# Kernel optimization log

Hardware: AMD Instinct MI355X
Metric: run time of the kernel (lower is better)

Reference implementation:

```python
import jax, jax.numpy as jnp
import numpy as np

DIM = 384
NH = 16
HD = DIM // NH          # 24
HID = DIM * 4           # titan/cms hidden
RD = 2 * (HD // 3 // 2) # 8 rope channels per axis (d/h/w), 3*RD == HD


def _ln(x, scale, bias):
    m = x.mean(-1, keepdims=True)
    v = ((x - m) ** 2).mean(-1, keepdims=True)
    return (x - m) * jax.lax.rsqrt(v + 1e-5) * scale + bias


def _mlp(x, w1, b1, w2, b2):
    # TitanMemory / CMS level: Linear -> GELU -> Linear (titan_layers=2)
    h = jax.nn.gelu(x @ w1 + b1, approximate=False)
    return h @ w2 + b2


def _rotate(x, pos):
    # rotate_queries_or_keys: interleaved rotary. x: [B,nh,N,d], pos: [N]
    d = x.shape[-1]
    inv_freq = 1.0 / (10000.0 ** (jnp.arange(0, d, 2, dtype=jnp.float32) / d))
    ang = pos[:, None] * inv_freq[None, :]              # [N, d/2]
    sin, cos = jnp.sin(ang), jnp.cos(ang)
    x1, x2 = x[..., 0::2], x[..., 1::2]
    y1 = x1 * cos - x2 * sin
    y2 = x1 * sin + x2 * cos
    return jnp.stack([y1, y2], axis=-1).reshape(x.shape)


def _rope3d(q, T, H, W):
    # 3D RoPE on frame tokens (action_tokens=0): time / height / width axes
    B, N, D = q.shape
    qh = q.reshape(B, N, NH, HD).transpose(0, 2, 1, 3)   # [B,nh,N,hd]
    ids = jnp.arange(T * H * W)
    tpos = (ids // (H * W)).astype(jnp.float32)
    hpos = ((ids % (H * W)) // W).astype(jnp.float32)
    wpos = (ids % W).astype(jnp.float32)
    qd = _rotate(qh[..., :RD], tpos)
    qhh = _rotate(qh[..., RD:2 * RD], hpos)
    qww = _rotate(qh[..., 2 * RD:3 * RD], wpos)
    out = jnp.concatenate([qd, qhh, qww], axis=-1)
    return out.transpose(0, 2, 1, 3).reshape(B, N, D)


def setup_inputs() -> dict:
    key = jax.random.key(0)
    ks = jax.random.split(key, 8)
    B, T, H, W = 8, 8, 16, 16
    N = T * H * W
    p = lambda k, sh: jax.random.normal(k, sh, jnp.float32) * 0.02
    return {
        "x": jax.random.normal(ks[0], (B, N, DIM), jnp.float32),
        "norm1_scale": jnp.ones((DIM,), jnp.float32),
        "norm1_bias": jnp.zeros((DIM,), jnp.float32),
        "norm2_scale": jnp.ones((DIM,), jnp.float32),
        "norm2_bias": jnp.zeros((DIM,), jnp.float32),
        "q_w": p(ks[1], (DIM, DIM)),
        # stacked Titan memories: [M_k, M_v, M_eta, M_alpha, M_memory]
        "titan_w1": p(ks[2], (5, DIM, HID)),
        "titan_b1": jnp.zeros((5, HID), jnp.float32),
        "titan_w2": p(ks[3], (5, HID, DIM)),
        "titan_b2": jnp.zeros((5, DIM), jnp.float32),
        "out_w": p(ks[4], (DIM, DIM)),
        "out_b": jnp.zeros((DIM,), jnp.float32),
        # CMS levels: [fast, medium, slow]
        "cms_w1": p(ks[5], (3, DIM, HID)),
        "cms_b1": jnp.zeros((3, HID), jnp.float32),
        "cms_w2": p(ks[6], (3, HID, DIM)),
        "cms_b2": jnp.zeros((3, DIM), jnp.float32),
        "T": T, "H": H, "W": W, "action_tokens": 0,
    }


def reference(x, norm1_scale, norm1_bias, norm2_scale, norm2_bias, q_w,
              titan_w1, titan_b1, titan_w2, titan_b2, out_w, out_b,
              cms_w1, cms_b1, cms_w2, cms_b2, T, H, W, action_tokens):
    # Phase A: self-modifying Titan (eval path: retrieval only)
    y = _ln(x, norm1_scale, norm1_bias)
    q = y @ q_w                                  # static query projection (Eq. 76)
    q = _rope3d(q, T, H, W)                      # 3D RoPE (action_tokens == 0)
    out = _mlp(q, titan_w1[4], titan_b1[4], titan_w2[4], titan_b2[4])  # M_memory(q)
    out = out @ out_w + out_b                    # out_proj
    x = x + out                                  # residual (drop_path = identity)
    # Phase B: CMS multi-frequency MLP cascade
    y = _ln(x, norm2_scale, norm2_bias)
    cms = sum(_mlp(y, cms_w1[i], cms_b1[i], cms_w2[i], cms_b2[i]) for i in range(3))
    return x + cms
```

## Files before the change

### kernel.cpp

```cpp
#include <hip/hip_runtime.h>
#include <math.h>

typedef unsigned short u16;
typedef unsigned int u32;
typedef __attribute__((ext_vector_type(8))) short short8;
typedef __attribute__((ext_vector_type(4))) float f32x4;

#define DIM 384
#define HID 1536

static __device__ __forceinline__ float bf2f(u32 b){ return __uint_as_float(b << 16); }
static __device__ __forceinline__ u16 f2bf(float f){
  u32 u = __float_as_uint(f);
  u32 r = (u + 0x7fffu + ((u >> 16) & 1u)) >> 16;
  return (u16)r;
}
static __device__ __forceinline__ float gelu_fast(float v){
  float u = v * fmaf(0.0713548162726f, v * v, 1.59576912161f);
  float e = __builtin_amdgcn_exp2f(-1.44269504089f * u);
  return v * __builtin_amdgcn_rcpf(1.0f + e);
}
static __device__ __forceinline__ void gload_lds16(const u16* g, u16* l){
  __builtin_amdgcn_global_load_lds(
      (__attribute__((address_space(1))) void*)(void*)const_cast<u16*>(g),
      (__attribute__((address_space(3))) void*)(void*)l, 16, 0, 0);
}

__global__ __launch_bounds__(256) void ln_kernel(const float* __restrict__ x,
    const float* __restrict__ sc, const float* __restrict__ bi, u16* __restrict__ y){
  int lane = threadIdx.x & 63;
  int row = blockIdx.x * 4 + (threadIdx.x >> 6);
  const float* xr = x + (size_t)row * DIM;
  float v[6];
  float s = 0.f, sq = 0.f;
#pragma unroll
  for (int i = 0; i < 6; ++i){
    float f = xr[lane + 64*i];
    v[i] = f; s += f; sq += f*f;
  }
#pragma unroll
  for (int o = 1; o < 64; o <<= 1){ s += __shfl_xor(s, o); sq += __shfl_xor(sq, o); }
  float mean = s * (1.0f/DIM);
  float var = sq * (1.0f/DIM) - mean*mean;
  float inv = rsqrtf(var + 1e-5f);
  u16* yr = y + (size_t)row * DIM;
#pragma unroll
  for (int i = 0; i < 6; ++i){
    int c = lane + 64*i;
    yr[c] = f2bf((v[i] - mean) * inv * sc[c] + bi[c]);
  }
}

__global__ __launch_bounds__(256) void rope_kernel(u16* __restrict__ q,
    const int* __restrict__ Tp, const int* __restrict__ Hp, const int* __restrict__ Wp,
    int Mtok){
  int idx = blockIdx.x * 256 + threadIdx.x;
  int tok = idx / 192;
  if (tok >= Mtok) return;
  int p = idx - tok * 192;
  int H = *Hp, W = *Wp, T = *Tp;
  int HW = H * W;
  int Ns = T * HW;
  int n = tok % Ns;
  int head = p / 12;
  int pp = p - head * 12;
  int s = pp >> 2, f = pp & 3;
  float pos;
  if (s == 0)      pos = (float)(n / HW);
  else if (s == 1) pos = (float)((n / W) % H);
  else             pos = (float)(n % W);
  const float LOG2_10000 = 13.28771237954945f;
  float inv = __builtin_amdgcn_exp2f(-0.25f * (float)f * LOG2_10000);
  float ang = pos * inv;
  float sn = __sinf(ang), cs = __cosf(ang);
  size_t base = (size_t)tok * DIM + head * 24 + s * 8 + 2 * f;
  u32 u = *(u32*)(q + base);
  float x1 = bf2f(u & 0xffffu), x2 = bf2f(u >> 16);
  float y1 = x1 * cs - x2 * sn;
  float y2 = x1 * sn + x2 * cs;
  *(u32*)(q + base) = (u32)f2bf(y1) | ((u32)f2bf(y2) << 16);
}

template<int R, int C>
__global__ __launch_bounds__(256) void transpose_kernel(
    const float* __restrict__ s0, const float* __restrict__ s1,
    const float* __restrict__ s2, const float* __restrict__ s3,
    u16* __restrict__ d0, u16* __restrict__ d1, u16* __restrict__ d2, u16* __restrict__ d3,
    int dstStride){
  const float* src = (blockIdx.z == 0) ? s0 : (blockIdx.z == 1) ? s1 : (blockIdx.z == 2) ? s2 : s3;
  u16* dst         = (blockIdx.z == 0) ? d0 : (blockIdx.z == 1) ? d1 : (blockIdx.z == 2) ? d2 : d3;
  __shared__ u16 t[32][33];
  int tx = threadIdx.x & 31, ty = threadIdx.x >> 5;
  int r0 = blockIdx.y * 32, c0 = blockIdx.x * 32;
#pragma unroll
  for (int i = 0; i < 4; ++i)
    t[ty + 8*i][tx] = f2bf(src[(size_t)(r0 + ty + 8*i) * C + c0 + tx]);
  __syncthreads();
#pragma unroll
  for (int i = 0; i < 4; ++i)
    dst[(size_t)(c0 + ty + 8*i) * dstStride + r0 + tx] = t[tx][ty + 8*i];
}

__global__ void bias3_kernel(const float* __restrict__ b, float* __restrict__ o){
  int n = threadIdx.x;
  o[n] = b[n] + b[384 + n] + b[768 + n];
}

enum { E_NONE = 0, E_BIAS = 1, E_RES_F32 = 3, E_FINAL = 5 };

template<int BM, int N, int K, int EPI>
__global__ __launch_bounds__(256) void gemm_kernel(
    const u16* __restrict__ A, const u16* __restrict__ Bt,
    void* __restrict__ Cv, const float* __restrict__ bias,
    const float* __restrict__ res, float* __restrict__ accbuf){
  constexpr int BN = 128, BK = 64;
  constexpr int MT = BM / 32, NT = 4;
  constexpr int AIT = BM / 32, BIT = 4;
  __shared__ __align__(16) u16 As[BM * BK];
  __shared__ __align__(16) u16 Bs[BN * BK];
  const int tid = threadIdx.x;
  const int lane = tid & 63;
  const int wv = tid >> 6;
  const int wm = (wv >> 1) * (BM / 2);
  const int wn = (wv & 1) * 64;
  const int quad = lane >> 4;
  const int l16 = lane & 15;
  const int rsw = l16 & 7;
  const size_t m0 = (size_t)blockIdx.x * BM;
  const int n0 = blockIdx.y * BN;
  const int srow = lane >> 3;
  const int scol = ((lane & 7) ^ srow) * 8;

  f32x4 acc[MT][NT];
  const f32x4 zero = {0.f, 0.f, 0.f, 0.f};
#pragma unroll
  for (int mt = 0; mt < MT; ++mt)
#pragma unroll
    for (int nt = 0; nt < NT; ++nt) acc[mt][nt] = zero;

  for (int kt = 0; kt < K; kt += BK){
#pragma unroll
    for (int i = 0; i < AIT; ++i){
      int seg = i * 4 + wv;
      gload_lds16(A + (m0 + (size_t)(seg * 8 + srow)) * K + kt + scol, As + seg * 512);
    }
#pragma unroll
    for (int i = 0; i < BIT; ++i){
      int seg = i * 4 + wv;
      gload_lds16(Bt + (size_t)(n0 + seg * 8 + srow) * K + kt + scol, Bs + seg * 512);
    }
    __syncthreads();
#pragma unroll
    for (int kk = 0; kk < 2; ++kk){
      short8 af[MT], bfr[NT];
#pragma unroll
      for (int mt = 0; mt < MT; ++mt)
        af[mt] = *(const short8*)(As + (wm + mt*16 + l16) * BK + (((kk*4 + quad) ^ rsw) << 3));
#pragma unroll
      for (int nt = 0; nt < NT; ++nt)
        bfr[nt] = *(const short8*)(Bs + (wn + nt*16 + l16) * BK + (((kk*4 + quad) ^ rsw) << 3));
#pragma unroll
      for (int mt = 0; mt < MT; ++mt)
#pragma unroll
        for (int nt = 0; nt < NT; ++nt)
          acc[mt][nt] = __builtin_amdgcn_mfma_f32_16x16x32_bf16(af[mt], bfr[nt], acc[mt][nt], 0, 0, 0);
    }
    __syncthreads();
  }

#pragma unroll
  for (int mt = 0; mt < MT; ++mt){
#pragma unroll
    for (int nt = 0; nt < NT; ++nt){
      int ncol = n0 + wn + nt*16 + l16;
      float bv = (EPI != E_NONE) ? bias[ncol] : 0.f;
      size_t mbase = m0 + wm + mt*16 + quad*4;
#pragma unroll
      for (int r = 0; r < 4; ++r){
        size_t off = (mbase + r) * N + ncol;
        float vv = acc[mt][nt][r];
        if      (EPI == E_NONE)      ((u16*)Cv)[off] = f2bf(vv);
        else if (EPI == E_BIAS)      ((u16*)Cv)[off] = f2bf(vv + bv);
        else          accbuf[off] = vv + bv + res[off];
      }
    }
  }
}

template<int N, int K>
__global__ __launch_bounds__(512, 4) void gemm_up2_kernel(
    const u16* __restrict__ A, const u16* __restrict__ Bt,
    u16* __restrict__ C, const float* __restrict__ bias){
  constexpr int BK = 64;
  __shared__ __align__(16) u16 As[128 * BK];
  __shared__ __align__(16) u16 Bs[256 * BK];
  const int tid = threadIdx.x;
  const int lane = tid & 63;
  const int wv = tid >> 6;
  const int wm = (wv >> 1) * 32;
  const int wn = (wv & 1) * 128;
  const int quad = lane >> 4;
  const int l16 = lane & 15;
  const int rsw = l16 & 7;
  const size_t m0 = (size_t)blockIdx.x * 128;
  const int n0 = blockIdx.y * 256;
  const int srow = lane >> 3;
  const int scol = ((lane & 7) ^ srow) * 8;

  f32x4 acc[2][8];
  const f32x4 zero = {0.f, 0.f, 0.f, 0.f};
#pragma unroll
  for (int mt = 0; mt < 2; ++mt)
#pragma unroll
    for (int nt = 0; nt < 8; ++nt) acc[mt][nt] = zero;

  for (int kt = 0; kt < K; kt += BK){
#pragma unroll
    for (int i = 0; i < 2; ++i){
      int seg = i * 8 + wv;
      gload_lds16(A + (m0 + (size_t)(seg * 8 + srow)) * K + kt + scol, As + seg * 512);
    }
#pragma unroll
    for (int i = 0; i < 4; ++i){
      int seg = i * 8 + wv;
      gload_lds16(Bt + (size_t)(n0 + seg * 8 + srow) * K + kt + scol, Bs + seg * 512);
    }
    __syncthreads();
#pragma unroll
    for (int kk = 0; kk < 2; ++kk){
      short8 af[2], bfr[8];
#pragma unroll
      for (int mt = 0; mt < 2; ++mt)
        af[mt] = *(const short8*)(As + (wm + mt*16 + l16) * BK + (((kk*4 + quad) ^ rsw) << 3));
#pragma unroll
      for (int nt = 0; nt < 8; ++nt)
        bfr[nt] = *(const short8*)(Bs + (wn + nt*16 + l16) * BK + (((kk*4 + quad) ^ rsw) << 3));
#pragma unroll
      for (int mt = 0; mt < 2; ++mt)
#pragma unroll
        for (int nt = 0; nt < 8; ++nt)
          acc[mt][nt] = __builtin_amdgcn_mfma_f32_16x16x32_bf16(af[mt], bfr[nt], acc[mt][nt], 0, 0, 0);
    }
    __syncthreads();
  }

#pragma unroll
  for (int mt = 0; mt < 2; ++mt){
#pragma unroll
    for (int nt = 0; nt < 8; ++nt){
      int ncol = n0 + wn + nt*16 + l16;
      float bv = bias[ncol];
      size_t mbase = m0 + wm + mt*16 + quad*4;
#pragma unroll
      for (int r = 0; r < 4; ++r)
        C[(mbase + r) * N + ncol] = f2bf(gelu_fast(acc[mt][nt][r] + bv));
    }
  }
}

template<int N, int K, int EPI>
__global__ __launch_bounds__(512, 4) void gemm2_kernel(
    const u16* __restrict__ A, const u16* __restrict__ Bt,
    void* __restrict__ Cv, const float* __restrict__ bias,
    const float* __restrict__ accbuf){
  constexpr int BK = 64;
  __shared__ __align__(16) u16 As[128 * BK];
  __shared__ __align__(16) u16 Bs[128 * BK];
  const int tid = threadIdx.x;
  const int lane = tid & 63;
  const int wv = tid >> 6;
  const int wm = (wv >> 1) * 32;
  const int wn = (wv & 1) * 64;
  const int quad = lane >> 4;
  const int l16 = lane & 15;
  const int rsw = l16 & 7;
  const size_t m0 = (size_t)blockIdx.x * 128;
  const int n0 = blockIdx.y * 128;
  const int srow = lane >> 3;
  const int scol = ((lane & 7) ^ srow) * 8;

  f32x4 acc[2][4];
  const f32x4 zero = {0.f, 0.f, 0.f, 0.f};
#pragma unroll
  for (int mt = 0; mt < 2; ++mt)
#pragma unroll
    for (int nt = 0; nt < 4; ++nt) acc[mt][nt] = zero;

  for (int kt = 0; kt < K; kt += BK){
#pragma unroll
    for (int i = 0; i < 2; ++i){
      int seg = i * 8 + wv;
      gload_lds16(A + (m0 + (size_t)(seg * 8 + srow)) * K + kt + scol, As + seg * 512);
      gload_lds16(Bt + (size_t)(n0 + seg * 8 + srow) * K + kt + scol, Bs + seg * 512);
    }
    __syncthreads();
#pragma unroll
    for (int kk = 0; kk < 2; ++kk){
      short8 af[2], bfr[4];
#pragma unroll
      for (int mt = 0; mt < 2; ++mt)
        af[mt] = *(const short8*)(As + (wm + mt*16 + l16) * BK + (((kk*4 + quad) ^ rsw) << 3));
#pragma unroll
      for (int nt = 0; nt < 4; ++nt)
        bfr[nt] = *(const short8*)(Bs + (wn + nt*16 + l16) * BK + (((kk*4 + quad) ^ rsw) << 3));
#pragma unroll
      for (int mt = 0; mt < 2; ++mt)
#pragma unroll
        for (int nt = 0; nt < 4; ++nt)
          acc[mt][nt] = __builtin_amdgcn_mfma_f32_16x16x32_bf16(af[mt], bfr[nt], acc[mt][nt], 0, 0, 0);
    }
    __syncthreads();
  }

#pragma unroll
  for (int mt = 0; mt < 2; ++mt){
#pragma unroll
    for (int nt = 0; nt < 4; ++nt){
      int ncol = n0 + wn + nt*16 + l16;
      float bv = bias[ncol];
      size_t mbase = m0 + wm + mt*16 + quad*4;
#pragma unroll
      for (int r = 0; r < 4; ++r){
        size_t off = (mbase + r) * N + ncol;
        float vv = acc[mt][nt][r] + bv;
        if (EPI == E_BIAS) ((u16*)Cv)[off] = f2bf(vv);
        else  ((float*)Cv)[off] = accbuf[off] + vv;
      }
    }
  }
}

extern "C" void kernel_launch(void* const* d_in, const int* in_sizes, int n_in,
                              void* d_out, int out_size, void* d_ws, size_t ws_size,
                              hipStream_t stream) {
  const int W11 = DIM * HID;
  const float* x   = (const float*)d_in[0];
  const float* n1s = (const float*)d_in[1];
  const float* n1b = (const float*)d_in[2];
  const float* n2s = (const float*)d_in[3];
  const float* n2b = (const float*)d_in[4];
  const float* qw  = (const float*)d_in[5];
  const float* tw1 = (const float*)d_in[6] + 4 * W11;
  const float* tb1 = (const float*)d_in[7] + 4 * HID;
  const float* tw2 = (const float*)d_in[8] + 4 * W11;
  const float* tb2 = (const float*)d_in[9] + 4 * DIM;
  const float* ow  = (const float*)d_in[10];
  const float* ob  = (const float*)d_in[11];
  const float* cw1 = (const float*)d_in[12];
  const float* cb1 = (const float*)d_in[13];
  const float* cw2 = (const float*)d_in[14];
  const float* cb2 = (const float*)d_in[15];
  const int* Tp = (const int*)d_in[16];
  const int* Hp = (const int*)d_in[17];
  const int* Wp = (const int*)d_in[18];
  const int M = in_sizes[0] / DIM;

  char* ws = (char*)d_ws;
  if (ws_size < 198772224u) return;
  u16*  y    = (u16*) (ws + 0);
  u16*  h    = (u16*) (ws + 12582912);
  float* x2  = (float*)(ws + 163577856);
  u16*  qwT  = (u16*) (ws + 188743680);
  u16*  owT  = (u16*) (ws + 189038592);
  u16*  w1T  = (u16*) (ws + 189333504);
  u16*  w2T  = (u16*) (ws + 190513152);
  u16*  cw1T = (u16*) (ws + 191692800);
  u16*  cw2T = (u16*) (ws + 195231744);
  float* cb2s = (float*)(ws + 198770688);
  u16*  qb   = (u16*)d_out;

  transpose_kernel<384,384><<<dim3(12,12,2),256,0,stream>>>(
      qw, ow, qw, qw, qwT, owT, qwT, qwT, 384);
  transpose_kernel<384,1536><<<dim3(48,12,4),256,0,stream>>>(
      tw1, cw1, cw1 + W11, cw1 + 2*W11, w1T, cw1T, cw1T + W11, cw1T + 2*W11, 384);
  transpose_kernel<1536,384><<<dim3(12,48,1),256,0,stream>>>(
      tw2, tw2, tw2, tw2, w2T, w2T, w2T, w2T, 1536);
  transpose_kernel<1536,384><<<dim3(12,48,3),256,0,stream>>>(
      cw2, cw2 + W11, cw2 + 2*W11, cw2, cw2T, cw2T + 1536, cw2T + 3072, cw2T, 4608);
  bias3_kernel<<<1,384,0,stream>>>(cb2, cb2s);

  ln_kernel<<<M/4,256,0,stream>>>(x, n1s, n1b, y);
  gemm_kernel<64,384,384,E_NONE><<<dim3(M/64,3),256,0,stream>>>(y, qwT, qb, nullptr, nullptr, nullptr);
  rope_kernel<<<(M*192)/256,256,0,stream>>>(qb, Tp, Hp, Wp, M);
  gemm_up2_kernel<1536,384><<<dim3(M/128,6),512,0,stream>>>(qb, w1T, h, tb1);
  gemm2_kernel<384,1536,E_BIAS><<<dim3(M/128,3),512,0,stream>>>(h, w2T, qb, tb2, nullptr);
  gemm_kernel<64,384,384,E_RES_F32><<<dim3(M/64,3),256,0,stream>>>(qb, owT, nullptr, ob, x, x2);
  ln_kernel<<<M/4,256,0,stream>>>(x2, n2s, n2b, y);
  gemm_up2_kernel<4608,384><<<dim3(M/128,18),512,0,stream>>>(y, cw1T, h, cb1);
  gemm2_kernel<384,4608,E_FINAL><<<dim3(M/128,3),512,0,stream>>>(h, cw2T, d_out, cb2s, x2);
}
```

Baseline: 394.1 us.

## Pack GELU outputs as bf16 pairs via permuted hidden layout; unify GEMM kernels

The up-projection epilogue now writes two adjacent bf16 GELU outputs per 32-bit store using v_cvt_pk_bf16_f32. This works because the hidden columns are interleaved, and the down-projection weight transposes apply a matching permutation on the K dimension. The 384x384 projections switch from the 64-row, 256-thread gemm_kernel to the 128-row, 512-thread gemm2_kernel, which gains extra epilogue modes. The aim is fewer, wider stores on the large hidden buffer and a single GEMM template, at the cost of a permuted weight layout that must stay consistent between the up and down kernels.

```diff
diff --git a/kernel.cpp b/kernel.cpp
--- a/kernel.cpp
+++ b/kernel.cpp
@@ -81,7 +81,7 @@
   *(u32*)(q + base) = (u32)f2bf(y1) | ((u32)f2bf(y2) << 16);
 }
 
-template<int R, int C>
+template<int R, int C, int PERM>
 __global__ __launch_bounds__(256) void transpose_kernel(
     const float* __restrict__ s0, const float* __restrict__ s1,
     const float* __restrict__ s2, const float* __restrict__ s3,
@@ -96,9 +96,10 @@
   for (int i = 0; i < 4; ++i)
     t[ty + 8*i][tx] = f2bf(src[(size_t)(r0 + ty + 8*i) * C + c0 + tx]);
   __syncthreads();
+  int txp = PERM ? (((tx & 15) << 1) | (tx >> 4)) : tx;
 #pragma unroll
   for (int i = 0; i < 4; ++i)
-    dst[(size_t)(c0 + ty + 8*i) * dstStride + r0 + tx] = t[tx][ty + 8*i];
+    dst[(size_t)(c0 + ty + 8*i) * dstStride + r0 + txp] = t[tx][ty + 8*i];
 }
 
 __global__ void bias3_kernel(const float* __restrict__ b, float* __restrict__ o){
@@ -108,80 +109,75 @@
 
 enum { E_NONE = 0, E_BIAS = 1, E_RES_F32 = 3, E_FINAL = 5 };
 
-template<int BM, int N, int K, int EPI>
-__global__ __launch_bounds__(256) void gemm_kernel(
+template<int N, int K, int EPI>
+__global__ __launch_bounds__(512, 4) void gemm2_kernel(
     const u16* __restrict__ A, const u16* __restrict__ Bt,
     void* __restrict__ Cv, const float* __restrict__ bias,
     const float* __restrict__ res, float* __restrict__ accbuf){
-  constexpr int BN = 128, BK = 64;
-  constexpr int MT = BM / 32, NT = 4;
-  constexpr int AIT = BM / 32, BIT = 4;
-  __shared__ __align__(16) u16 As[BM * BK];
-  __shared__ __align__(16) u16 Bs[BN * BK];
+  constexpr int BK = 64;
+  __shared__ __align__(16) u16 As[128 * BK];
+  __shared__ __align__(16) u16 Bs[128 * BK];
   const int tid = threadIdx.x;
   const int lane = tid & 63;
   const int wv = tid >> 6;
-  const int wm = (wv >> 1) * (BM / 2);
+  const int wm = (wv >> 1) * 32;
   const int wn = (wv & 1) * 64;
   const int quad = lane >> 4;
   const int l16 = lane & 15;
   const int rsw = l16 & 7;
-  const size_t m0 = (size_t)blockIdx.x * BM;
-  const int n0 = blockIdx.y * BN;
+  const size_t m0 = (size_t)blockIdx.x * 128;
+  const int n0 = blockIdx.y * 128;
   const int srow = lane >> 3;
   const int scol = ((lane & 7) ^ srow) * 8;
 
-  f32x4 acc[MT][NT];
+  f32x4 acc[2][4];
   const f32x4 zero = {0.f, 0.f, 0.f, 0.f};
 #pragma unroll
-  for (int mt = 0; mt < MT; ++mt)
-#pragma unroll
-    for (int nt = 0; nt < NT; ++nt) acc[mt][nt] = zero;
+  for (int mt = 0; mt < 2; ++mt)
+#pragma unroll
+    for (int nt = 0; nt < 4; ++nt) acc[mt][nt] = zero;
 
   for (int kt = 0; kt < K; kt += BK){
 #pragma unroll
-    for (int i = 0; i < AIT; ++i){
-      int seg = i * 4 + wv;
+    for (int i = 0; i < 2; ++i){
+      int seg = i * 8 + wv;
       gload_lds16(A + (m0 + (size_t)(seg * 8 + srow)) * K + kt + scol, As + seg * 512);
-    }
-#pragma unroll
-    for (int i = 0; i < BIT; ++i){
-      int seg = i * 4 + wv;
       gload_lds16(Bt + (size_t)(n0 + seg * 8 + srow) * K + kt + scol, Bs + seg * 512);
     }
     __syncthreads();
 #pragma unroll
     for (int kk = 0; kk < 2; ++kk){
-      short8 af[MT], bfr[NT];
-#pragma unroll
-      for (int mt = 0; mt < MT; ++mt)
+      short8 af[2], bfr[4];
+#pragma unroll
+      for (int mt = 0; mt < 2; ++mt)
         af[mt] = *(const short8*)(As + (wm + mt*16 + l16) * BK + (((kk*4 + quad) ^ rsw) << 3));
 #pragma unroll
-      for (int nt = 0; nt < NT; ++nt)
+      for (int nt = 0; nt < 4; ++nt)
         bfr[nt] = *(const short8*)(Bs + (wn + nt*16 + l16) * BK + (((kk*4 + quad) ^ rsw) << 3));
 #pragma unroll
-      for (int mt = 0; mt < MT; ++mt)
-#pragma unroll
-        for (int nt = 0; nt < NT; ++nt)
+      for (int mt = 0; mt < 2; ++mt)
+#pragma unroll
+        for (int nt = 0; nt < 4; ++nt)
           acc[mt][nt] = __builtin_amdgcn_mfma_f32_16x16x32_bf16(af[mt], bfr[nt], acc[mt][nt], 0, 0, 0);
     }
     __syncthreads();
   }
 
 #pragma unroll
-  for (int mt = 0; mt < MT; ++mt){
-#pragma unroll
-    for (int nt = 0; nt < NT; ++nt){
+  for (int mt = 0; mt < 2; ++mt){
+#pragma unroll
+    for (int nt = 0; nt < 4; ++nt){
       int ncol = n0 + wn + nt*16 + l16;
       float bv = (EPI != E_NONE) ? bias[ncol] : 0.f;
       size_t mbase = m0 + wm + mt*16 + quad*4;
 #pragma unroll
       for (int r = 0; r < 4; ++r){
         size_t off = (mbase + r) * N + ncol;
-        float vv = acc[mt][nt][r];
-        if      (EPI == E_NONE)      ((u16*)Cv)[off] = f2bf(vv);
-        else if (EPI == E_BIAS)      ((u16*)Cv)[off] = f2bf(vv + bv);
-        else          accbuf[off] = vv + bv + res[off];
+        float vv = acc[mt][nt][r] + bv;
+        if      (EPI == E_NONE)    ((u16*)Cv)[off] = f2bf(vv);
+        else if (EPI == E_BIAS)    ((u16*)Cv)[off] = f2bf(vv);
+        else if (EPI == E_RES_F32) accbuf[off] = vv + res[off];
+        else          ((float*)Cv)[off] = accbuf[off] + vv;
       }
     }
   }
@@ -247,84 +243,19 @@
 #pragma unroll
   for (int mt = 0; mt < 2; ++mt){
 #pragma unroll
-    for (int nt = 0; nt < 8; ++nt){
-      int ncol = n0 + wn + nt*16 + l16;
-      float bv = bias[ncol];
+    for (int j = 0; j < 4; ++j){
+      int g32 = n0 + wn + j*32;
+      float bv0 = bias[g32 + l16];
+      float bv1 = bias[g32 + 16 + l16];
       size_t mbase = m0 + wm + mt*16 + quad*4;
-#pragma unroll
-      for (int r = 0; r < 4; ++r)
-        C[(mbase + r) * N + ncol] = f2bf(gelu_fast(acc[mt][nt][r] + bv));
-    }
-  }
-}
-
-template<int N, int K, int EPI>
-__global__ __launch_bounds__(512, 4) void gemm2_kernel(
-    const u16* __restrict__ A, const u16* __restrict__ Bt,
-    void* __restrict__ Cv, const float* __restrict__ bias,
-    const float* __restrict__ accbuf){
-  constexpr int BK = 64;
-  __shared__ __align__(16) u16 As[128 * BK];
-  __shared__ __align__(16) u16 Bs[128 * BK];
-  const int tid = threadIdx.x;
-  const int lane = tid & 63;
-  const int wv = tid >> 6;
-  const int wm = (wv >> 1) * 32;
-  const int wn = (wv & 1) * 64;
-  const int quad = lane >> 4;
-  const int l16 = lane & 15;
-  const int rsw = l16 & 7;
-  const size_t m0 = (size_t)blockIdx.x * 128;
-  const int n0 = blockIdx.y * 128;
-  const int srow = lane >> 3;
-  const int scol = ((lane & 7) ^ srow) * 8;
-
-  f32x4 acc[2][4];
-  const f32x4 zero = {0.f, 0.f, 0.f, 0.f};
-#pragma unroll
-  for (int mt = 0; mt < 2; ++mt)
-#pragma unroll
-    for (int nt = 0; nt < 4; ++nt) acc[mt][nt] = zero;
-
-  for (int kt = 0; kt < K; kt += BK){
-#pragma unroll
-    for (int i = 0; i < 2; ++i){
-      int seg = i * 8 + wv;
-      gload_lds16(A + (m0 + (size_t)(seg * 8 + srow)) * K + kt + scol, As + seg * 512);
-      gload_lds16(Bt + (size_t)(n0 + seg * 8 + srow) * K + kt + scol, Bs + seg * 512);
-    }
-    __syncthreads();
-#pragma unroll
-    for (int kk = 0; kk < 2; ++kk){
-      short8 af[2], bfr[4];
-#pragma unroll
-      for (int mt = 0; mt < 2; ++mt)
-        af[mt] = *(const short8*)(As + (wm + mt*16 + l16) * BK + (((kk*4 + quad) ^ rsw) << 3));
-#pragma unroll
-      for (int nt = 0; nt < 4; ++nt)
-        bfr[nt] = *(const short8*)(Bs + (wn + nt*16 + l16) * BK + (((kk*4 + quad) ^ rsw) << 3));
-#pragma unroll
-      for (int mt = 0; mt < 2; ++mt)
-#pragma unroll
-        for (int nt = 0; nt < 4; ++nt)
-          acc[mt][nt] = __builtin_amdgcn_mfma_f32_16x16x32_bf16(af[mt], bfr[nt], acc[mt][nt], 0, 0, 0);
-    }
-    __syncthreads();
-  }
-
-#pragma unroll
-  for (int mt = 0; mt < 2; ++mt){
-#pragma unroll
-    for (int nt = 0; nt < 4; ++nt){
-      int ncol = n0 + wn + nt*16 + l16;
-      float bv = bias[ncol];
-      size_t mbase = m0 + wm + mt*16 + quad*4;
+      size_t cb = (size_t)g32 + 2*l16;
 #pragma unroll
       for (int r = 0; r < 4; ++r){
-        size_t off = (mbase + r) * N + ncol;
-        float vv = acc[mt][nt][r] + bv;
-        if (EPI == E_BIAS) ((u16*)Cv)[off] = f2bf(vv);
-        else  ((float*)Cv)[off] = accbuf[off] + vv;
+        float g0 = gelu_fast(acc[mt][2*j][r] + bv0);
+        float g1 = gelu_fast(acc[mt][2*j+1][r] + bv1);
+        u32 pk;
+        asm("v_cvt_pk_bf16_f32 %0, %1, %2" : "=v"(pk) : "v"(g0), "v"(g1));
+        *(u32*)(C + (mbase + r) * N + cb) = pk;
       }
     }
   }
@@ -369,23 +300,27 @@
   float* cb2s = (float*)(ws + 198770688);
   u16*  qb   = (u16*)d_out;
 
-  transpose_kernel<384,384><<<dim3(12,12,2),256,0,stream>>>(
+  transpose_kernel<384,384,0><<<dim3(12,12,2),256,0,stream>>>(
       qw, ow, qw, qw, qwT, owT, qwT, qwT, 384);
-  transpose_kernel<384,1536><<<dim3(48,12,4),256,0,stream>>>(
+  transpose_kernel<384,1536,0><<<dim3(48,12,4),256,0,stream>>>(
       tw1, cw1, cw1 + W11, cw1 + 2*W11, w1T, cw1T, cw1T + W11, cw1T + 2*W11, 384);
-  transpose_kernel<1536,384><<<dim3(12,48,1),256,0,stream>>>(
+  transpose_kernel<1536,384,1><<<dim3(12,48,1),256,0,stream>>>(
       tw2, tw2, tw2, tw2, w2T, w2T, w2T, w2T, 1536);
-  transpose_kernel<1536,384><<<dim3(12,48,3),256,0,stream>>>(
+  transpose_kernel<1536,384,1><<<dim3(12,48,3),256,0,stream>>>(
       cw2, cw2 + W11, cw2 + 2*W11, cw2, cw2T, cw2T + 1536, cw2T + 3072, cw2T, 4608);
   bias3_kernel<<<1,384,0,stream>>>(cb2, cb2s);
 
   ln_kernel<<<M/4,256,0,stream>>>(x, n1s, n1b, y);
-  gemm_kernel<64,384,384,E_NONE><<<dim3(M/64,3),256,0,stream>>>(y, qwT, qb, nullptr, nullptr, nullptr);
+  gemm2_kernel<384,384,E_NONE><<<dim3(M/128,3),512,0,stream>>>(
+      y, qwT, qb, nullptr, nullptr, nullptr);
   rope_kernel<<<(M*192)/256,256,0,stream>>>(qb, Tp, Hp, Wp, M);
   gemm_up2_kernel<1536,384><<<dim3(M/128,6),512,0,stream>>>(qb, w1T, h, tb1);
-  gemm2_kernel<384,1536,E_BIAS><<<dim3(M/128,3),512,0,stream>>>(h, w2T, qb, tb2, nullptr);
-  gemm_kernel<64,384,384,E_RES_F32><<<dim3(M/64,3),256,0,stream>>>(qb, owT, nullptr, ob, x, x2);
+  gemm2_kernel<384,1536,E_BIAS><<<dim3(M/128,3),512,0,stream>>>(
+      h, w2T, qb, tb2, nullptr, nullptr);
+  gemm2_kernel<384,384,E_RES_F32><<<dim3(M/128,3),512,0,stream>>>(
+      qb, owT, nullptr, ob, x, x2);
   ln_kernel<<<M/4,256,0,stream>>>(x2, n2s, n2b, y);
   gemm_up2_kernel<4608,384><<<dim3(M/128,18),512,0,stream>>>(y, cw1T, h, cb1);
-  gemm2_kernel<384,4608,E_FINAL><<<dim3(M/128,3),512,0,stream>>>(h, cw2T, d_out, cb2s, x2);
-}
+  gemm2_kernel<384,4608,E_FINAL><<<dim3(M/128,3),512,0,stream>>>(
+      h, cw2T, d_out, cb2s, nullptr, x2);
+}
```

Measured after the change: 418.2 us. 1.06x slower.

## Split-K the final CMS down-projection with atomics and pack GELU stores

Applied to the files above, without the earlier changes.

The final 4608-deep down-projection is split into two K halves that atomically add into the output. The output is pre-initialised by the out-proj epilogue with residual plus summed CMS bias, which doubles the grid of that low-occupancy GEMM. The up-projection epilogue now writes packed pairs of bf16 values via v_cvt_pk_bf16_f32. To keep the result correct, the down-projection weight transposes permute columns to match the packed hidden layout. The cost is nondeterministic float summation order and an extra fp32 output write in the out-proj GEMM.

```diff
diff --git a/kernel.cpp b/kernel.cpp
--- a/kernel.cpp
+++ b/kernel.cpp
@@ -81,7 +81,7 @@
   *(u32*)(q + base) = (u32)f2bf(y1) | ((u32)f2bf(y2) << 16);
 }
 
-template<int R, int C>
+template<int R, int C, int PERM>
 __global__ __launch_bounds__(256) void transpose_kernel(
     const float* __restrict__ s0, const float* __restrict__ s1,
     const float* __restrict__ s2, const float* __restrict__ s3,
@@ -96,9 +96,10 @@
   for (int i = 0; i < 4; ++i)
     t[ty + 8*i][tx] = f2bf(src[(size_t)(r0 + ty + 8*i) * C + c0 + tx]);
   __syncthreads();
+  int txp = PERM ? (((tx & 15) << 1) | (tx >> 4)) : tx;
 #pragma unroll
   for (int i = 0; i < 4; ++i)
-    dst[(size_t)(c0 + ty + 8*i) * dstStride + r0 + tx] = t[tx][ty + 8*i];
+    dst[(size_t)(c0 + ty + 8*i) * dstStride + r0 + txp] = t[tx][ty + 8*i];
 }
 
 __global__ void bias3_kernel(const float* __restrict__ b, float* __restrict__ o){
@@ -106,13 +107,14 @@
   o[n] = b[n] + b[384 + n] + b[768 + n];
 }
 
-enum { E_NONE = 0, E_BIAS = 1, E_RES_F32 = 3, E_FINAL = 5 };
+enum { E_NONE = 0, E_BIAS = 1, E_RES_DUAL = 2 };
 
 template<int BM, int N, int K, int EPI>
 __global__ __launch_bounds__(256) void gemm_kernel(
     const u16* __restrict__ A, const u16* __restrict__ Bt,
     void* __restrict__ Cv, const float* __restrict__ bias,
-    const float* __restrict__ res, float* __restrict__ accbuf){
+    const float* __restrict__ res, float* __restrict__ accbuf,
+    const float* __restrict__ bias2){
   constexpr int BN = 128, BK = 64;
   constexpr int MT = BM / 32, NT = 4;
   constexpr int AIT = BM / 32, BIT = 4;
@@ -174,15 +176,153 @@
     for (int nt = 0; nt < NT; ++nt){
       int ncol = n0 + wn + nt*16 + l16;
       float bv = (EPI != E_NONE) ? bias[ncol] : 0.f;
+      float bv2 = (EPI == E_RES_DUAL) ? bias2[ncol] : 0.f;
       size_t mbase = m0 + wm + mt*16 + quad*4;
 #pragma unroll
       for (int r = 0; r < 4; ++r){
         size_t off = (mbase + r) * N + ncol;
         float vv = acc[mt][nt][r];
-        if      (EPI == E_NONE)      ((u16*)Cv)[off] = f2bf(vv);
-        else if (EPI == E_BIAS)      ((u16*)Cv)[off] = f2bf(vv + bv);
-        else          accbuf[off] = vv + bv + res[off];
+        if (EPI == E_NONE) ((u16*)Cv)[off] = f2bf(vv);
+        else {
+          float t = vv + bv + res[off];
+          accbuf[off] = t;
+          ((float*)Cv)[off] = t + bv2;
+        }
       }
+    }
+  }
+}
+
+template<int N, int K>
+__global__ __launch_bounds__(512, 4) void gemm2_kernel(
+    const u16* __restrict__ A, const u16* __restrict__ Bt,
+    u16* __restrict__ C, const float* __restrict__ bias){
+  constexpr int BK = 64;
+  __shared__ __align__(16) u16 As[128 * BK];
+  __shared__ __align__(16) u16 Bs[128 * BK];
+  const int tid = threadIdx.x;
+  const int lane = tid & 63;
+  const int wv = tid >> 6;
+  const int wm = (wv >> 1) * 32;
+  const int wn = (wv & 1) * 64;
+  const int quad = lane >> 4;
+  const int l16 = lane & 15;
+  const int rsw = l16 & 7;
+  const size_t m0 = (size_t)blockIdx.x * 128;
+  const int n0 = blockIdx.y * 128;
+  const int srow = lane >> 3;
+  const int scol = ((lane & 7) ^ srow) * 8;
+
+  f32x4 acc[2][4];
+  const f32x4 zero = {0.f, 0.f, 0.f, 0.f};
+#pragma unroll
+  for (int mt = 0; mt < 2; ++mt)
+#pragma unroll
+    for (int nt = 0; nt < 4; ++nt) acc[mt][nt] = zero;
+
+  for (int kt = 0; kt < K; kt += BK){
+#pragma unroll
+    for (int i = 0; i < 2; ++i){
+      int seg = i * 8 + wv;
+      gload_lds16(A + (m0 + (size_t)(seg * 8 + srow)) * K + kt + scol, As + seg * 512);
+      gload_lds16(Bt + (size_t)(n0 + seg * 8 + srow) * K + kt + scol, Bs + seg * 512);
+    }
+    __syncthreads();
+#pragma unroll
+    for (int kk = 0; kk < 2; ++kk){
+      short8 af[2], bfr[4];
+#pragma unroll
+      for (int mt = 0; mt < 2; ++mt)
+        af[mt] = *(const short8*)(As + (wm + mt*16 + l16) * BK + (((kk*4 + quad) ^ rsw) << 3));
+#pragma unroll
+      for (int nt = 0; nt < 4; ++nt)
+        bfr[nt] = *(const short8*)(Bs + (wn + nt*16 + l16) * BK + (((kk*4 + quad) ^ rsw) << 3));
+#pragma unroll
+      for (int mt = 0; mt < 2; ++mt)
+#pragma unroll
+        for (int nt = 0; nt < 4; ++nt)
+          acc[mt][nt] = __builtin_amdgcn_mfma_f32_16x16x32_bf16(af[mt], bfr[nt], acc[mt][nt], 0, 0, 0);
+    }
+    __syncthreads();
+  }
+
+#pragma unroll
+  for (int mt = 0; mt < 2; ++mt){
+#pragma unroll
+    for (int nt = 0; nt < 4; ++nt){
+      int ncol = n0 + wn + nt*16 + l16;
+      float bv = bias[ncol];
+      size_t mbase = m0 + wm + mt*16 + quad*4;
+#pragma unroll
+      for (int r = 0; r < 4; ++r)
+        C[(mbase + r) * N + ncol] = f2bf(acc[mt][nt][r] + bv);
+    }
+  }
+}
+
+template<int N, int K, int KC>
+__global__ __launch_bounds__(512, 4) void gemm2_atomic_kernel(
+    const u16* __restrict__ A, const u16* __restrict__ Bt,
+    float* __restrict__ out){
+  constexpr int BK = 64;
+  __shared__ __align__(16) u16 As[128 * BK];
+  __shared__ __align__(16) u16 Bs[128 * BK];
+  const int tid = threadIdx.x;
+  const int lane = tid & 63;
+  const int wv = tid >> 6;
+  const int wm = (wv >> 1) * 32;
+  const int wn = (wv & 1) * 64;
+  const int quad = lane >> 4;
+  const int l16 = lane & 15;
+  const int rsw = l16 & 7;
+  const size_t m0 = (size_t)blockIdx.x * 128;
+  const int n0 = blockIdx.y * 128;
+  const int k0 = blockIdx.z * KC;
+  const int srow = lane >> 3;
+  const int scol = ((lane & 7) ^ srow) * 8;
+
+  f32x4 acc[2][4];
+  const f32x4 zero = {0.f, 0.f, 0.f, 0.f};
+#pragma unroll
+  for (int mt = 0; mt < 2; ++mt)
+#pragma unroll
+    for (int nt = 0; nt < 4; ++nt) acc[mt][nt] = zero;
+
+  for (int kt = k0; kt < k0 + KC; kt += BK){
+#pragma unroll
+    for (int i = 0; i < 2; ++i){
+      int seg = i * 8 + wv;
+      gload_lds16(A + (m0 + (size_t)(seg * 8 + srow)) * K + kt + scol, As + seg * 512);
+      gload_lds16(Bt + (size_t)(n0 + seg * 8 + srow) * K + kt + scol, Bs + seg * 512);
+    }
+    __syncthreads();
+#pragma unroll
+    for (int kk = 0; kk < 2; ++kk){
+      short8 af[2], bfr[4];
+#pragma unroll
+      for (int mt = 0; mt < 2; ++mt)
+        af[mt] = *(const short8*)(As + (wm + mt*16 + l16) * BK + (((kk*4 + quad) ^ rsw) << 3));
+#pragma unroll
+      for (int nt = 0; nt < 4; ++nt)
+        bfr[nt] = *(const short8*)(Bs + (wn + nt*16 + l16) * BK + (((kk*4 + quad) ^ rsw) << 3));
+#pragma unroll
+      for (int mt = 0; mt < 2; ++mt)
+#pragma unroll
+        for (int nt = 0; nt < 4; ++nt)
+          acc[mt][nt] = __builtin_amdgcn_mfma_f32_16x16x32_bf16(af[mt], bfr[nt], acc[mt][nt], 0, 0, 0);
+    }
+    __syncthreads();
+  }
+
+#pragma unroll
+  for (int mt = 0; mt < 2; ++mt){
+#pragma unroll
+    for (int nt = 0; nt < 4; ++nt){
+      int ncol = n0 + wn + nt*16 + l16;
+      size_t mbase = m0 + wm + mt*16 + quad*4;
+#pragma unroll
+      for (int r = 0; r < 4; ++r)
+        unsafeAtomicAdd(out + (mbase + r) * N + ncol, acc[mt][nt][r]);
     }
   }
 }
@@ -247,84 +387,19 @@
 #pragma unroll
   for (int mt = 0; mt < 2; ++mt){
 #pragma unroll
-    for (int nt = 0; nt < 8; ++nt){
-      int ncol = n0 + wn + nt*16 + l16;
-      float bv = bias[ncol];
+    for (int j = 0; j < 4; ++j){
+      int g32 = n0 + wn + j*32;
+      float bv0 = bias[g32 + l16];
+      float bv1 = bias[g32 + 16 + l16];
       size_t mbase = m0 + wm + mt*16 + quad*4;
-#pragma unroll
-      for (int r = 0; r < 4; ++r)
-        C[(mbase + r) * N + ncol] = f2bf(gelu_fast(acc[mt][nt][r] + bv));
-    }
-  }
-}
-
-template<int N, int K, int EPI>
-__global__ __launch_bounds__(512, 4) void gemm2_kernel(
-    const u16* __restrict__ A, const u16* __restrict__ Bt,
-    void* __restrict__ Cv, const float* __restrict__ bias,
-    const float* __restrict__ accbuf){
-  constexpr int BK = 64;
-  __shared__ __align__(16) u16 As[128 * BK];
-  __shared__ __align__(16) u16 Bs[128 * BK];
-  const int tid = threadIdx.x;
-  const int lane = tid & 63;
-  const int wv = tid >> 6;
-  const int wm = (wv >> 1) * 32;
-  const int wn = (wv & 1) * 64;
-  const int quad = lane >> 4;
-  const int l16 = lane & 15;
-  const int rsw = l16 & 7;
-  const size_t m0 = (size_t)blockIdx.x * 128;
-  const int n0 = blockIdx.y * 128;
-  const int srow = lane >> 3;
-  const int scol = ((lane & 7) ^ srow) * 8;
-
-  f32x4 acc[2][4];
-  const f32x4 zero = {0.f, 0.f, 0.f, 0.f};
-#pragma unroll
-  for (int mt = 0; mt < 2; ++mt)
-#pragma unroll
-    for (int nt = 0; nt < 4; ++nt) acc[mt][nt] = zero;
-
-  for (int kt = 0; kt < K; kt += BK){
-#pragma unroll
-    for (int i = 0; i < 2; ++i){
-      int seg = i * 8 + wv;
-      gload_lds16(A + (m0 + (size_t)(seg * 8 + srow)) * K + kt + scol, As + seg * 512);
-      gload_lds16(Bt + (size_t)(n0 + seg * 8 + srow) * K + kt + scol, Bs + seg * 512);
-    }
-    __syncthreads();
-#pragma unroll
-    for (int kk = 0; kk < 2; ++kk){
-      short8 af[2], bfr[4];
-#pragma unroll
-      for (int mt = 0; mt < 2; ++mt)
-        af[mt] = *(const short8*)(As + (wm + mt*16 + l16) * BK + (((kk*4 + quad) ^ rsw) << 3));
-#pragma unroll
-      for (int nt = 0; nt < 4; ++nt)
-        bfr[nt] = *(const short8*)(Bs + (wn + nt*16 + l16) * BK + (((kk*4 + quad) ^ rsw) << 3));
-#pragma unroll
-      for (int mt = 0; mt < 2; ++mt)
-#pragma unroll
-        for (int nt = 0; nt < 4; ++nt)
-          acc[mt][nt] = __builtin_amdgcn_mfma_f32_16x16x32_bf16(af[mt], bfr[nt], acc[mt][nt], 0, 0, 0);
-    }
-    __syncthreads();
-  }
-
-#pragma unroll
-  for (int mt = 0; mt < 2; ++mt){
-#pragma unroll
-    for (int nt = 0; nt < 4; ++nt){
-      int ncol = n0 + wn + nt*16 + l16;
-      float bv = bias[ncol];
-      size_t mbase = m0 + wm + mt*16 + quad*4;
+      size_t cb = (size_t)g32 + 2*l16;
 #pragma unroll
       for (int r = 0; r < 4; ++r){
-        size_t off = (mbase + r) * N + ncol;
-        float vv = acc[mt][nt][r] + bv;
-        if (EPI == E_BIAS) ((u16*)Cv)[off] = f2bf(vv);
-        else  ((float*)Cv)[off] = accbuf[off] + vv;
+        float g0 = gelu_fast(acc[mt][2*j][r] + bv0);
+        float g1 = gelu_fast(acc[mt][2*j+1][r] + bv1);
+        u32 pk;
+        asm("v_cvt_pk_bf16_f32 %0, %1, %2" : "=v"(pk) : "v"(g0), "v"(g1));
+        *(u32*)(C + (mbase + r) * N + cb) = pk;
       }
     }
   }
@@ -369,23 +444,26 @@
   float* cb2s = (float*)(ws + 198770688);
   u16*  qb   = (u16*)d_out;
 
-  transpose_kernel<384,384><<<dim3(12,12,2),256,0,stream>>>(
+  transpose_kernel<384,384,0><<<dim3(12,12,2),256,0,stream>>>(
       qw, ow, qw, qw, qwT, owT, qwT, qwT, 384);
-  transpose_kernel<384,1536><<<dim3(48,12,4),256,0,stream>>>(
+  transpose_kernel<384,1536,0><<<dim3(48,12,4),256,0,stream>>>(
       tw1, cw1, cw1 + W11, cw1 + 2*W11, w1T, cw1T, cw1T + W11, cw1T + 2*W11, 384);
-  transpose_kernel<1536,384><<<dim3(12,48,1),256,0,stream>>>(
+  transpose_kernel<1536,384,1><<<dim3(12,48,1),256,0,stream>>>(
       tw2, tw2, tw2, tw2, w2T, w2T, w2T, w2T, 1536);
-  transpose_kernel<1536,384><<<dim3(12,48,3),256,0,stream>>>(
+  transpose_kernel<1536,384,1><<<dim3(12,48,3),256,0,stream>>>(
       cw2, cw2 + W11, cw2 + 2*W11, cw2, cw2T, cw2T + 1536, cw2T + 3072, cw2T, 4608);
   bias3_kernel<<<1,384,0,stream>>>(cb2, cb2s);
 
   ln_kernel<<<M/4,256,0,stream>>>(x, n1s, n1b, y);
-  gemm_kernel<64,384,384,E_NONE><<<dim3(M/64,3),256,0,stream>>>(y, qwT, qb, nullptr, nullptr, nullptr);
+  gemm_kernel<64,384,384,E_NONE><<<dim3(M/64,3),256,0,stream>>>(
+      y, qwT, qb, nullptr, nullptr, nullptr, nullptr);
   rope_kernel<<<(M*192)/256,256,0,stream>>>(qb, Tp, Hp, Wp, M);
   gemm_up2_kernel<1536,384><<<dim3(M/128,6),512,0,stream>>>(qb, w1T, h, tb1);
-  gemm2_kernel<384,1536,E_BIAS><<<dim3(M/128,3),512,0,stream>>>(h, w2T, qb, tb2, nullptr);
-  gemm_kernel<64,384,384,E_RES_F32><<<dim3(M/64,3),256,0,stream>>>(qb, owT, nullptr, ob, x, x2);
+  gemm2_kernel<384,1536><<<dim3(M/128,3),512,0,stream>>>(h, w2T, y, tb2);
+  gemm_kernel<64,384,384,E_RES_DUAL><<<dim3(M/64,3),256,0,stream>>>(
+      y, owT, d_out, ob, x, x2, cb2s);
   ln_kernel<<<M/4,256,0,stream>>>(x2, n2s, n2b, y);
   gemm_up2_kernel<4608,384><<<dim3(M/128,18),512,0,stream>>>(y, cw1T, h, cb1);
-  gemm2_kernel<384,4608,E_FINAL><<<dim3(M/128,3),512,0,stream>>>(h, cw2T, d_out, cb2s, x2);
-}
+  gemm2_atomic_kernel<384,4608,2304><<<dim3(M/128,3,2),512,0,stream>>>(
+      h, cw2T, (float*)d_out);
+}
```

Result: slower. 433.3 us (+10.0%).

## Split-K CMS down-projection with atomics and pre-seeded output, packed GELU stores

Applied to the files above, without the earlier changes.

The CMS down-projection becomes a split-K kernel over two K halves. Each block covers all 384 output columns for 64 rows and atomically adds its partial sums into the output. The out-proj epilogue now writes both x2 and x2 plus the summed CMS bias into the output, so the atomics accumulate onto that seed. The up-projection stores GELU results as packed bf16 pairs, made valid by permuting the columns of the down weight transposes. The Titan down GEMM moves to the 64-row gemm_kernel, buffers are reused, and fp32 atomics add contention and non-deterministic summation order.

```diff
diff --git a/kernel.cpp b/kernel.cpp
--- a/kernel.cpp
+++ b/kernel.cpp
@@ -81,7 +81,7 @@
   *(u32*)(q + base) = (u32)f2bf(y1) | ((u32)f2bf(y2) << 16);
 }
 
-template<int R, int C>
+template<int R, int C, int PERM>
 __global__ __launch_bounds__(256) void transpose_kernel(
     const float* __restrict__ s0, const float* __restrict__ s1,
     const float* __restrict__ s2, const float* __restrict__ s3,
@@ -96,9 +96,10 @@
   for (int i = 0; i < 4; ++i)
     t[ty + 8*i][tx] = f2bf(src[(size_t)(r0 + ty + 8*i) * C + c0 + tx]);
   __syncthreads();
+  int txp = PERM ? (((tx & 15) << 1) | (tx >> 4)) : tx;
 #pragma unroll
   for (int i = 0; i < 4; ++i)
-    dst[(size_t)(c0 + ty + 8*i) * dstStride + r0 + tx] = t[tx][ty + 8*i];
+    dst[(size_t)(c0 + ty + 8*i) * dstStride + r0 + txp] = t[tx][ty + 8*i];
 }
 
 __global__ void bias3_kernel(const float* __restrict__ b, float* __restrict__ o){
@@ -106,13 +107,14 @@
   o[n] = b[n] + b[384 + n] + b[768 + n];
 }
 
-enum { E_NONE = 0, E_BIAS = 1, E_RES_F32 = 3, E_FINAL = 5 };
+enum { E_NONE = 0, E_BIAS = 1, E_RES_DUAL = 2 };
 
 template<int BM, int N, int K, int EPI>
 __global__ __launch_bounds__(256) void gemm_kernel(
     const u16* __restrict__ A, const u16* __restrict__ Bt,
     void* __restrict__ Cv, const float* __restrict__ bias,
-    const float* __restrict__ res, float* __restrict__ accbuf){
+    const float* __restrict__ res, float* __restrict__ accbuf,
+    const float* __restrict__ bias2){
   constexpr int BN = 128, BK = 64;
   constexpr int MT = BM / 32, NT = 4;
   constexpr int AIT = BM / 32, BIT = 4;
@@ -174,15 +176,85 @@
     for (int nt = 0; nt < NT; ++nt){
       int ncol = n0 + wn + nt*16 + l16;
       float bv = (EPI != E_NONE) ? bias[ncol] : 0.f;
+      float bv2 = (EPI == E_RES_DUAL) ? bias2[ncol] : 0.f;
       size_t mbase = m0 + wm + mt*16 + quad*4;
 #pragma unroll
       for (int r = 0; r < 4; ++r){
         size_t off = (mbase + r) * N + ncol;
         float vv = acc[mt][nt][r];
-        if      (EPI == E_NONE)      ((u16*)Cv)[off] = f2bf(vv);
-        else if (EPI == E_BIAS)      ((u16*)Cv)[off] = f2bf(vv + bv);
-        else          accbuf[off] = vv + bv + res[off];
+        if      (EPI == E_NONE) ((u16*)Cv)[off] = f2bf(vv);
+        else if (EPI == E_BIAS) ((u16*)Cv)[off] = f2bf(vv + bv);
+        else {
+          float t = vv + bv + res[off];
+          accbuf[off] = t;
+          ((float*)Cv)[off] = t + bv2;
+        }
       }
+    }
+  }
+}
+
+template<int N, int K, int KC>
+__global__ __launch_bounds__(512, 4) void gemm_down3_kernel(
+    const u16* __restrict__ A, const u16* __restrict__ Bt,
+    float* __restrict__ out){
+  constexpr int BK = 64;
+  __shared__ __align__(16) u16 As[64 * BK];
+  __shared__ __align__(16) u16 Bs[384 * BK];
+  const int tid = threadIdx.x;
+  const int lane = tid & 63;
+  const int wv = tid >> 6;
+  const int quad = lane >> 4;
+  const int l16 = lane & 15;
+  const int rsw = l16 & 7;
+  const size_t m0 = (size_t)blockIdx.x * 64;
+  const int k0 = blockIdx.z * KC;
+  const int srow = lane >> 3;
+  const int scol = ((lane & 7) ^ srow) * 8;
+  const int dwn = wv * 48;
+
+  f32x4 acc[4][3];
+  const f32x4 zero = {0.f, 0.f, 0.f, 0.f};
+#pragma unroll
+  for (int mt = 0; mt < 4; ++mt)
+#pragma unroll
+    for (int nt = 0; nt < 3; ++nt) acc[mt][nt] = zero;
+
+  for (int kt = k0; kt < k0 + KC; kt += BK){
+    gload_lds16(A + (m0 + (size_t)(wv * 8 + srow)) * K + kt + scol, As + wv * 512);
+#pragma unroll
+    for (int i = 0; i < 6; ++i){
+      int seg = i * 8 + wv;
+      gload_lds16(Bt + (size_t)(seg * 8 + srow) * K + kt + scol, Bs + seg * 512);
+    }
+    __syncthreads();
+#pragma unroll
+    for (int kk = 0; kk < 2; ++kk){
+      short8 af[4], bfr[3];
+#pragma unroll
+      for (int mt = 0; mt < 4; ++mt)
+        af[mt] = *(const short8*)(As + (mt*16 + l16) * BK + (((kk*4 + quad) ^ rsw) << 3));
+#pragma unroll
+      for (int nt = 0; nt < 3; ++nt)
+        bfr[nt] = *(const short8*)(Bs + (dwn + nt*16 + l16) * BK + (((kk*4 + quad) ^ rsw) << 3));
+#pragma unroll
+      for (int mt = 0; mt < 4; ++mt)
+#pragma unroll
+        for (int nt = 0; nt < 3; ++nt)
+          acc[mt][nt] = __builtin_amdgcn_mfma_f32_16x16x32_bf16(af[mt], bfr[nt], acc[mt][nt], 0, 0, 0);
+    }
+    __syncthreads();
+  }
+
+#pragma unroll
+  for (int mt = 0; mt < 4; ++mt){
+#pragma unroll
+    for (int nt = 0; nt < 3; ++nt){
+      int ncol = dwn + nt*16 + l16;
+      size_t mbase = m0 + mt*16 + quad*4;
+#pragma unroll
+      for (int r = 0; r < 4; ++r)
+        unsafeAtomicAdd(out + (mbase + r) * N + ncol, acc[mt][nt][r]);
     }
   }
 }
@@ -247,84 +319,19 @@
 #pragma unroll
   for (int mt = 0; mt < 2; ++mt){
 #pragma unroll
-    for (int nt = 0; nt < 8; ++nt){
-      int ncol = n0 + wn + nt*16 + l16;
-      float bv = bias[ncol];
+    for (int j = 0; j < 4; ++j){
+      int g32 = n0 + wn + j*32;
+      float bv0 = bias[g32 + l16];
+      float bv1 = bias[g32 + 16 + l16];
       size_t mbase = m0 + wm + mt*16 + quad*4;
-#pragma unroll
-      for (int r = 0; r < 4; ++r)
-        C[(mbase + r) * N + ncol] = f2bf(gelu_fast(acc[mt][nt][r] + bv));
-    }
-  }
-}
-
-template<int N, int K, int EPI>
-__global__ __launch_bounds__(512, 4) void gemm2_kernel(
-    const u16* __restrict__ A, const u16* __restrict__ Bt,
-    void* __restrict__ Cv, const float* __restrict__ bias,
-    const float* __restrict__ accbuf){
-  constexpr int BK = 64;
-  __shared__ __align__(16) u16 As[128 * BK];
-  __shared__ __align__(16) u16 Bs[128 * BK];
-  const int tid = threadIdx.x;
-  const int lane = tid & 63;
-  const int wv = tid >> 6;
-  const int wm = (wv >> 1) * 32;
-  const int wn = (wv & 1) * 64;
-  const int quad = lane >> 4;
-  const int l16 = lane & 15;
-  const int rsw = l16 & 7;
-  const size_t m0 = (size_t)blockIdx.x * 128;
-  const int n0 = blockIdx.y * 128;
-  const int srow = lane >> 3;
-  const int scol = ((lane & 7) ^ srow) * 8;
-
-  f32x4 acc[2][4];
-  const f32x4 zero = {0.f, 0.f, 0.f, 0.f};
-#pragma unroll
-  for (int mt = 0; mt < 2; ++mt)
-#pragma unroll
-    for (int nt = 0; nt < 4; ++nt) acc[mt][nt] = zero;
-
-  for (int kt = 0; kt < K; kt += BK){
-#pragma unroll
-    for (int i = 0; i < 2; ++i){
-      int seg = i * 8 + wv;
-      gload_lds16(A + (m0 + (size_t)(seg * 8 + srow)) * K + kt + scol, As + seg * 512);
-      gload_lds16(Bt + (size_t)(n0 + seg * 8 + srow) * K + kt + scol, Bs + seg * 512);
-    }
-    __syncthreads();
-#pragma unroll
-    for (int kk = 0; kk < 2; ++kk){
-      short8 af[2], bfr[4];
-#pragma unroll
-      for (int mt = 0; mt < 2; ++mt)
-        af[mt] = *(const short8*)(As + (wm + mt*16 + l16) * BK + (((kk*4 + quad) ^ rsw) << 3));
-#pragma unroll
-      for (int nt = 0; nt < 4; ++nt)
-        bfr[nt] = *(const short8*)(Bs + (wn + nt*16 + l16) * BK + (((kk*4 + quad) ^ rsw) << 3));
-#pragma unroll
-      for (int mt = 0; mt < 2; ++mt)
-#pragma unroll
-        for (int nt = 0; nt < 4; ++nt)
-          acc[mt][nt] = __builtin_amdgcn_mfma_f32_16x16x32_bf16(af[mt], bfr[nt], acc[mt][nt], 0, 0, 0);
-    }
-    __syncthreads();
-  }
-
-#pragma unroll
-  for (int mt = 0; mt < 2; ++mt){
-#pragma unroll
-    for (int nt = 0; nt < 4; ++nt){
-      int ncol = n0 + wn + nt*16 + l16;
-      float bv = bias[ncol];
-      size_t mbase = m0 + wm + mt*16 + quad*4;
+      size_t cb = (size_t)g32 + 2*l16;
 #pragma unroll
       for (int r = 0; r < 4; ++r){
-        size_t off = (mbase + r) * N + ncol;
-        float vv = acc[mt][nt][r] + bv;
-        if (EPI == E_BIAS) ((u16*)Cv)[off] = f2bf(vv);
-        else  ((float*)Cv)[off] = accbuf[off] + vv;
+        float g0 = gelu_fast(acc[mt][2*j][r] + bv0);
+        float g1 = gelu_fast(acc[mt][2*j+1][r] + bv1);
+        u32 pk;
+        asm("v_cvt_pk_bf16_f32 %0, %1, %2" : "=v"(pk) : "v"(g0), "v"(g1));
+        *(u32*)(C + (mbase + r) * N + cb) = pk;
       }
     }
   }
@@ -369,23 +376,27 @@
   float* cb2s = (float*)(ws + 198770688);
   u16*  qb   = (u16*)d_out;
 
-  transpose_kernel<384,384><<<dim3(12,12,2),256,0,stream>>>(
+  transpose_kernel<384,384,0><<<dim3(12,12,2),256,0,stream>>>(
       qw, ow, qw, qw, qwT, owT, qwT, qwT, 384);
-  transpose_kernel<384,1536><<<dim3(48,12,4),256,0,stream>>>(
+  transpose_kernel<384,1536,0><<<dim3(48,12,4),256,0,stream>>>(
       tw1, cw1, cw1 + W11, cw1 + 2*W11, w1T, cw1T, cw1T + W11, cw1T + 2*W11, 384);
-  transpose_kernel<1536,384><<<dim3(12,48,1),256,0,stream>>>(
+  transpose_kernel<1536,384,1><<<dim3(12,48,1),256,0,stream>>>(
       tw2, tw2, tw2, tw2, w2T, w2T, w2T, w2T, 1536);
-  transpose_kernel<1536,384><<<dim3(12,48,3),256,0,stream>>>(
+  transpose_kernel<1536,384,1><<<dim3(12,48,3),256,0,stream>>>(
       cw2, cw2 + W11, cw2 + 2*W11, cw2, cw2T, cw2T + 1536, cw2T + 3072, cw2T, 4608);
   bias3_kernel<<<1,384,0,stream>>>(cb2, cb2s);
 
   ln_kernel<<<M/4,256,0,stream>>>(x, n1s, n1b, y);
-  gemm_kernel<64,384,384,E_NONE><<<dim3(M/64,3),256,0,stream>>>(y, qwT, qb, nullptr, nullptr, nullptr);
+  gemm_kernel<64,384,384,E_NONE><<<dim3(M/64,3),256,0,stream>>>(
+      y, qwT, qb, nullptr, nullptr, nullptr, nullptr);
   rope_kernel<<<(M*192)/256,256,0,stream>>>(qb, Tp, Hp, Wp, M);
   gemm_up2_kernel<1536,384><<<dim3(M/128,6),512,0,stream>>>(qb, w1T, h, tb1);
-  gemm2_kernel<384,1536,E_BIAS><<<dim3(M/128,3),512,0,stream>>>(h, w2T, qb, tb2, nullptr);
-  gemm_kernel<64,384,384,E_RES_F32><<<dim3(M/64,3),256,0,stream>>>(qb, owT, nullptr, ob, x, x2);
+  gemm_kernel<64,384,1536,E_BIAS><<<dim3(M/64,3),256,0,stream>>>(
+      h, w2T, y, tb2, nullptr, nullptr, nullptr);
+  gemm_kernel<64,384,384,E_RES_DUAL><<<dim3(M/64,3),256,0,stream>>>(
+      y, owT, d_out, ob, x, x2, cb2s);
   ln_kernel<<<M/4,256,0,stream>>>(x2, n2s, n2b, y);
   gemm_up2_kernel<4608,384><<<dim3(M/128,18),512,0,stream>>>(y, cw1T, h, cb1);
-  gemm2_kernel<384,4608,E_FINAL><<<dim3(M/128,3),512,0,stream>>>(h, cw2T, d_out, cb2s, x2);
-}
+  gemm_down3_kernel<384,4608,2304><<<dim3(M/64,1,2),512,0,stream>>>(
+      h, cw2T, (float*)d_out);
+}
```

After: 454.9 us. +15.4%, slower.
